# Performance work log

Hardware: AMD Instinct MI355X
Metric: run time of the kernel (lower is better)

The kernel has to match this reference:

```python
import jax, jax.numpy as jnp
import numpy as np

B, N, D, G = 128, 36, 512, 2  # batch, num_bboxs, wrd_embed_size, num_glimpses
NEG = -1e10


def setup_inputs() -> dict:
    key = jax.random.key(0)
    k1, k2, k3 = jax.random.split(key, 3)
    obj_repr = jax.random.normal(k1, (B, N, D), dtype=jnp.float32)
    # attn_glimpse[0]: nn.Linear(num_bboxs * wrd_embed_size, num_glimpses)
    W = jax.random.normal(k2, (G, N * D), dtype=jnp.float32) * 0.02
    b = jnp.zeros((G,), dtype=jnp.float32)
    bboxs_mask = jax.random.randint(k3, (B, N), 0, 2).astype(bool)
    bboxs_mask = bboxs_mask.at[:, 0].set(True)  # at least one valid box per row
    return {"obj_repr": obj_repr, "W": W, "b": b, "bboxs_mask": bboxs_mask}


def reference(obj_repr, W, b, bboxs_mask):
    """Faithful port of QGenModel.self_diff_attention."""
    Bv, Nv, Dv = obj_repr.shape
    # pairwise object differences, gated by the query object: [B, N, N, D]
    diff = obj_repr[:, :, None, :] * (obj_repr[:, :, None, :] - obj_repr[:, None, :, :])
    flat = diff.reshape(Bv, Nv, Nv * Dv)              # [B, N, N*D]
    logits = flat @ W.T + b                            # [B, N, G]
    logits = jnp.where(bboxs_mask[:, :, None], logits, NEG)
    weight = jax.nn.softmax(logits, axis=1)            # softmax over box axis (dim=1)
    # weight.transpose(1,2) @ obj_repr  ->  [B, G, D]
    vis_repr = jnp.einsum('bng,bnd->bgd', weight, obj_repr)
    return vis_repr.reshape(Bv, -1)                    # [B, G*D]
```

## Files before the change

### kernel.cpp

```cpp
#include <hip/hip_runtime.h>
#include <hip/hip_bf16.h>


#define QB 128
#define QN 36
#define QD 512
#define QG 2

__global__ __launch_bounds__(QD) void qgen_self_diff_attn(
    const float* __restrict__ obj,
    const float* __restrict__ W,
    const float* __restrict__ bias,
    const int* __restrict__ mask,
    float* __restrict__ out)
{
    __shared__ float s_T[QD];
    __shared__ float s_S[QD];
    __shared__ float s_logit[QN];
    __shared__ float s_w[QN];

    const int bid = blockIdx.x;
    const int b = bid & (QB - 1);
    const int g = bid >> 7;
    const int t = threadIdx.x;
    const int wave = t >> 6;
    const int lane = t & 63;

    const float* ob = obj + (size_t)b * QN * QD;
    const float* wg = W + (size_t)g * QN * QD;

    float o[QN];
    float T = 0.f, S = 0.f;
    #pragma unroll
    for (int m = 0; m < QN; ++m) {
        o[m] = ob[m * QD + t];
        float w = wg[m * QD + t];
        T = fmaf(w, o[m], T);
        S += w;
    }
    s_T[t] = T;
    s_S[t] = S;
    __syncthreads();

    for (int n = wave; n < QN; n += 8) {
        float a = 0.f;
        #pragma unroll
        for (int k = 0; k < QD / 64; ++k) {
            int d = lane + k * 64;
            float ov = ob[n * QD + d];
            a += ov * ov * s_S[d] - ov * s_T[d];
        }
        #pragma unroll
        for (int off = 32; off; off >>= 1)
            a += __shfl_down(a, off);
        if (lane == 0) {
            bool mk = mask[b * QN + n] != 0;
            s_logit[n] = mk ? a + bias[g] : -1e10f;
        }
    }
    __syncthreads();

    if (wave == 0) {
        float v = (lane < QN) ? s_logit[lane] : -1e30f;
        float mx = v;
        #pragma unroll
        for (int off = 32; off; off >>= 1)
            mx = fmaxf(mx, __shfl_xor(mx, off));
        float e = (lane < QN) ? __expf(v - mx) : 0.f;
        float sum = e;
        #pragma unroll
        for (int off = 32; off; off >>= 1)
            sum += __shfl_xor(sum, off);
        if (lane < QN) s_w[lane] = e / sum;
    }
    __syncthreads();

    float v = 0.f;
    #pragma unroll
    for (int n = 0; n < QN; ++n)
        v = fmaf(s_w[n], o[n], v);
    out[(size_t)b * QG * QD + (size_t)g * QD + t] = v;
}

extern "C" void kernel_launch(void* const* d_in, const int* in_sizes, int n_in,
                              void* d_out, int out_size, void* d_ws, size_t ws_size,
                              hipStream_t stream) {
    const float* obj  = (const float*)d_in[0];
    const float* W    = (const float*)d_in[1];
    const float* bias = (const float*)d_in[2];
    const int*   mask = (const int*)d_in[3];
    float* out = (float*)d_out;

    qgen_self_diff_attn<<<QB * QG, QD, 0, stream>>>(obj, W, bias, mask, out);
}
```

Measured before the change: 67.57 us.

## Use float4 row-split layout so each object row is loaded once

Each thread now owns a 4-wide column slice and a quarter of the object rows, held as float4 in registers. T/S partials are reduced across row groups through shared memory. The logit pass reuses the register-held rows instead of reloading obj from global memory. The weighted-sum output is reduced in shared memory and written as float4. This removes the second global read of obj and moves to vectorized loads, at the cost of extra shared-memory reductions and barriers.

```diff
diff --git a/kernel.cpp b/kernel.cpp
--- a/kernel.cpp
+++ b/kernel.cpp
@@ -6,16 +6,20 @@
 #define QN 36
 #define QD 512
 #define QG 2
+#define NROW 9
 
-__global__ __launch_bounds__(QD) void qgen_self_diff_attn(
+__global__ __launch_bounds__(512) void qgen_self_diff_attn(
     const float* __restrict__ obj,
     const float* __restrict__ W,
     const float* __restrict__ bias,
     const int* __restrict__ mask,
     float* __restrict__ out)
 {
+    __shared__ float4 s_p4[4][128];
+    __shared__ float4 s_q4[4][128];
     __shared__ float s_T[QD];
     __shared__ float s_S[QD];
+    __shared__ float s_pp[8][NROW];
     __shared__ float s_logit[QN];
     __shared__ float s_w[QN];
 
@@ -23,44 +27,67 @@
     const int b = bid & (QB - 1);
     const int g = bid >> 7;
     const int t = threadIdx.x;
-    const int wave = t >> 6;
+    const int w = t >> 6;
     const int lane = t & 63;
+    const int mq = t >> 7;
+    const int dq = t & 127;
 
-    const float* ob = obj + (size_t)b * QN * QD;
-    const float* wg = W + (size_t)g * QN * QD;
+    const float4* ob4 = (const float4*)(obj + (size_t)b * QN * QD);
+    const float4* wg4 = (const float4*)(W + (size_t)g * QN * QD);
 
-    float o[QN];
-    float T = 0.f, S = 0.f;
+    float4 o4[NROW];
+    float4 T4 = make_float4(0.f, 0.f, 0.f, 0.f);
+    float4 S4 = make_float4(0.f, 0.f, 0.f, 0.f);
     #pragma unroll
-    for (int m = 0; m < QN; ++m) {
-        o[m] = ob[m * QD + t];
-        float w = wg[m * QD + t];
-        T = fmaf(w, o[m], T);
-        S += w;
+    for (int i = 0; i < NROW; ++i) {
+        int m = mq + 4 * i;
+        float4 o = ob4[m * 128 + dq];
+        float4 wv = wg4[m * 128 + dq];
+        o4[i] = o;
+        T4.x = fmaf(wv.x, o.x, T4.x);  T4.y = fmaf(wv.y, o.y, T4.y);
+        T4.z = fmaf(wv.z, o.z, T4.z);  T4.w = fmaf(wv.w, o.w, T4.w);
+        S4.x += wv.x;  S4.y += wv.y;  S4.z += wv.z;  S4.w += wv.w;
     }
-    s_T[t] = T;
-    s_S[t] = S;
+    s_p4[mq][dq] = T4;
+    s_q4[mq][dq] = S4;
     __syncthreads();
 
-    for (int n = wave; n < QN; n += 8) {
-        float a = 0.f;
+    {
+        const float* fT = (const float*)s_p4;
+        const float* fS = (const float*)s_q4;
+        s_T[t] = fT[0 * QD + t] + fT[1 * QD + t] + fT[2 * QD + t] + fT[3 * QD + t];
+        s_S[t] = fS[0 * QD + t] + fS[1 * QD + t] + fS[2 * QD + t] + fS[3 * QD + t];
+    }
+    __syncthreads();
+
+    {
+        float4 ST = ((const float4*)s_T)[dq];
+        float4 SS = ((const float4*)s_S)[dq];
         #pragma unroll
-        for (int k = 0; k < QD / 64; ++k) {
-            int d = lane + k * 64;
-            float ov = ob[n * QD + d];
-            a += ov * ov * s_S[d] - ov * s_T[d];
-        }
-        #pragma unroll
-        for (int off = 32; off; off >>= 1)
-            a += __shfl_down(a, off);
-        if (lane == 0) {
-            bool mk = mask[b * QN + n] != 0;
-            s_logit[n] = mk ? a + bias[g] : -1e10f;
+        for (int i = 0; i < NROW; ++i) {
+            float4 o = o4[i];
+            float a = (o.x * o.x) * SS.x - o.x * ST.x
+                    + (o.y * o.y) * SS.y - o.y * ST.y
+                    + (o.z * o.z) * SS.z - o.z * ST.z
+                    + (o.w * o.w) * SS.w - o.w * ST.w;
+            #pragma unroll
+            for (int off = 32; off; off >>= 1)
+                a += __shfl_down(a, off);
+            if (lane == 0) s_pp[w][i] = a;
         }
     }
     __syncthreads();
 
-    if (wave == 0) {
+    if (t < QN) {
+        int n = t;
+        int nmq = n & 3, ni = n >> 2;
+        float a = s_pp[2 * nmq][ni] + s_pp[2 * nmq + 1][ni];
+        bool mk = mask[b * QN + n] != 0;
+        s_logit[n] = mk ? a + bias[g] : -1e10f;
+    }
+    __syncthreads();
+
+    if (w == 0) {
         float v = (lane < QN) ? s_logit[lane] : -1e30f;
         float mx = v;
         #pragma unroll
@@ -75,11 +102,29 @@
     }
     __syncthreads();
 
-    float v = 0.f;
-    #pragma unroll
-    for (int n = 0; n < QN; ++n)
-        v = fmaf(s_w[n], o[n], v);
-    out[(size_t)b * QG * QD + (size_t)g * QD + t] = v;
+    {
+        float4 v4 = make_float4(0.f, 0.f, 0.f, 0.f);
+        #pragma unroll
+        for (int i = 0; i < NROW; ++i) {
+            float wn = s_w[mq + 4 * i];
+            v4.x = fmaf(wn, o4[i].x, v4.x);
+            v4.y = fmaf(wn, o4[i].y, v4.y);
+            v4.z = fmaf(wn, o4[i].z, v4.z);
+            v4.w = fmaf(wn, o4[i].w, v4.w);
+        }
+        s_p4[mq][dq] = v4;
+    }
+    __syncthreads();
+
+    if (t < 128) {
+        float4 a = s_p4[0][t], b4 = s_p4[1][t], c = s_p4[2][t], d = s_p4[3][t];
+        float4 r;
+        r.x = a.x + b4.x + c.x + d.x;
+        r.y = a.y + b4.y + c.y + d.y;
+        r.z = a.z + b4.z + c.z + d.z;
+        r.w = a.w + b4.w + c.w + d.w;
+        ((float4*)out)[(size_t)b * (QG * QD / 4) + g * (QD / 4) + t] = r;
+    }
 }
 
 extern "C" void kernel_launch(void* const* d_in, const int* in_sizes, int n_in,
@@ -91,5 +136,5 @@
     const int*   mask = (const int*)d_in[3];
     float* out = (float*)d_out;
 
-    qgen_self_diff_attn<<<QB * QG, QD, 0, stream>>>(obj, W, bias, mask, out);
+    qgen_self_diff_attn<<<QB * QG, 512, 0, stream>>>(obj, W, bias, mask, out);
 }
```

Result: no change. 67.59 us (+0.0%).
